# Performance work log

Hardware: AMD Instinct MI355X
Metric: run time of the kernel (lower is better)

Reference implementation:

```python
import jax, jax.numpy as jnp
import numpy as np

D_MODEL = 512
NUM_HEADS = 8
HEAD_DIM = D_MODEL // NUM_HEADS
WINDOW = 64


def setup_inputs() -> dict:
    key = jax.random.key(0)
    ks = jax.random.split(key, 9)
    B, S = 2, 4096
    s = 1.0 / np.sqrt(D_MODEL)
    x = jax.random.normal(ks[0], (B, S, D_MODEL), dtype=jnp.float32)
    Wq = jax.random.uniform(ks[1], (D_MODEL, D_MODEL), jnp.float32, -s, s)
    bq = jax.random.uniform(ks[2], (D_MODEL,), jnp.float32, -s, s)
    Wk = jax.random.uniform(ks[3], (D_MODEL, D_MODEL), jnp.float32, -s, s)
    bk = jax.random.uniform(ks[4], (D_MODEL,), jnp.float32, -s, s)
    Wv = jax.random.uniform(ks[5], (D_MODEL, D_MODEL), jnp.float32, -s, s)
    bv = jax.random.uniform(ks[6], (D_MODEL,), jnp.float32, -s, s)
    Wo = jax.random.uniform(ks[7], (D_MODEL, D_MODEL), jnp.float32, -s, s)
    bo = jax.random.uniform(ks[8], (D_MODEL,), jnp.float32, -s, s)
    return {"x": x, "Wq": Wq, "bq": bq, "Wk": Wk, "bk": bk,
            "Wv": Wv, "bv": bv, "Wo": Wo, "bo": bo}


def reference(x, Wq, bq, Wk, bk, Wv, bv, Wo, bo):
    B, S, _ = x.shape
    # projections (torch Linear: x @ W.T + b)
    q = (x @ Wq.T + bq).reshape(B, S, NUM_HEADS, HEAD_DIM).transpose(0, 2, 1, 3)
    k = (x @ Wk.T + bk).reshape(B, S, NUM_HEADS, HEAD_DIM).transpose(0, 2, 1, 3)
    v = (x @ Wv.T + bv).reshape(B, S, NUM_HEADS, HEAD_DIM).transpose(0, 2, 1, 3)
    scores = jnp.einsum('bhqd,bhkd->bhqk', q, k) / jnp.sqrt(
        jnp.asarray(HEAD_DIM, x.dtype))
    idx = jnp.arange(S)
    local = jnp.abs(idx[None, :] - idx[:, None]) <= WINDOW  # [S,S]
    scores = jnp.where(local[None, None], scores, -jnp.inf)
    attn = jax.nn.softmax(scores, axis=-1)
    out = jnp.einsum('bhqk,bhkd->bhqd', attn, v)
    out = out.transpose(0, 2, 1, 3).reshape(B, S, D_MODEL)
    return out @ Wo.T + bo
```

## Files before the change

### kernel.cpp

```cpp
#include <hip/hip_runtime.h>
#include <hip/hip_bf16.h>

typedef __attribute__((ext_vector_type(8))) short short8;
typedef __attribute__((ext_vector_type(4))) short s16x4;
typedef __attribute__((ext_vector_type(4))) float f32x4;

#define S_LEN 4096
#define DM 512
#define NH 8
#define HD 64
#define NB 2

__device__ __forceinline__ ushort f2bf(float f) {
    union { float f; unsigned int i; } x; x.f = f;
    unsigned int i = x.i;
    unsigned int r = (i + 0x7fffu + ((i >> 16) & 1u)) >> 16;
    return (ushort)r;
}

__device__ __forceinline__ void gload16(const ushort* g, ushort* l) {
    __builtin_amdgcn_global_load_lds(
        (const __attribute__((address_space(1))) unsigned int*)(g),
        (__attribute__((address_space(3))) unsigned int*)(l),
        16, 0, 0);
}

__device__ __forceinline__ f32x4 mfma16(s16x4 a, s16x4 b, f32x4 c) {
#if __has_builtin(__builtin_amdgcn_mfma_f32_16x16x16bf16_1k)
    return __builtin_amdgcn_mfma_f32_16x16x16bf16_1k(a, b, c, 0, 0, 0);
#else
    f32x4 d;
    asm volatile("v_mfma_f32_16x16x16_bf16 %0, %1, %2, %3"
                 : "=v"(d) : "v"(a), "v"(b), "v"(c));
    return d;
#endif
}

__global__ __launch_bounds__(256) void cvt_all_kernel(
    const float* __restrict__ x,
    const float* __restrict__ s0, const float* __restrict__ s1,
    const float* __restrict__ s2, const float* __restrict__ s3,
    ushort* __restrict__ xb,
    ushort* __restrict__ t0, ushort* __restrict__ t1,
    ushort* __restrict__ t2, ushort* __restrict__ t3)
{
    const float* src;
    ushort* dst;
    size_t i;
    if (blockIdx.x < 2048) {
        src = x; dst = xb;
        i = (size_t)blockIdx.x * 256 + threadIdx.x;
    } else {
        const int wb = blockIdx.x - 2048;
        const int which = wb >> 7;
        src = (which == 0) ? s0 : (which == 1) ? s1 : (which == 2) ? s2 : s3;
        dst = (which == 0) ? t0 : (which == 1) ? t1 : (which == 2) ? t2 : t3;
        i = (size_t)(wb & 127) * 256 + threadIdx.x;
    }
    const float4* s = (const float4*)src;
    float4 a = s[i * 2], b = s[i * 2 + 1];
    short8 o;
    o[0] = (short)f2bf(a.x); o[1] = (short)f2bf(a.y);
    o[2] = (short)f2bf(a.z); o[3] = (short)f2bf(a.w);
    o[4] = (short)f2bf(b.x); o[5] = (short)f2bf(b.y);
    o[6] = (short)f2bf(b.z); o[7] = (short)f2bf(b.w);
    *(short8*)(dst + i * 8) = o;
}

__global__ __launch_bounds__(256) void qkv_proj_kernel(
    const ushort* __restrict__ X,
    const ushort* __restrict__ Wq, const float* __restrict__ bq,
    const ushort* __restrict__ Wk, const float* __restrict__ bk,
    const ushort* __restrict__ Wv, const float* __restrict__ bv,
    ushort* __restrict__ Qws, ushort* __restrict__ Kws, ushort* __restrict__ Vt)
{
    __shared__ __align__(1024) ushort As[128 * 64];
    __shared__ __align__(1024) ushort Bs[128 * 64];

    const int lane = threadIdx.x & 63;
    const int w    = threadIdx.x >> 6;
    const int xcd  = blockIdx.x & 7;
    const int idx  = blockIdx.x >> 3;
    const int tr   = xcd + 8 * (idx / 12);
    const int tc   = idx % 12;
    const int which = tc >> 2;
    const int c0   = (tc & 3) * 128;
    const int r0   = tr * 128;

    const ushort* W    = (which == 0) ? Wq : (which == 1) ? Wk : Wv;
    const float*  bias = (which == 0) ? bq : (which == 1) ? bk : bv;

    const int lr = lane & 15;
    const int lg = lane >> 4;
    const int wr = w >> 1, wc = w & 1;
    const int ldrow = lane >> 3;
    const int ldcol = (lane & 7) * 8;

    f32x4 acc[4][4] = {};
    for (int ks = 0; ks < 8; ks++) {
        const int k0 = ks * 64;
        if (ks) __syncthreads();
        const ushort* gA = X + (size_t)(r0 + ldrow) * DM + k0 + ldcol;
        const ushort* gB = W + (size_t)(c0 + ldrow) * DM + k0 + ldcol;
#pragma unroll
        for (int j = 0; j < 4; j++) {
            const int ch = w * 4 + j;
            gload16(gA + (size_t)ch * 8 * DM, As + ch * 512);
            gload16(gB + (size_t)ch * 8 * DM, Bs + ch * 512);
        }
        __syncthreads();

#pragma unroll
        for (int kk = 0; kk < 2; kk++) {
            const int koff = kk * 32 + lg * 8;
            short8 a[4], b[4];
#pragma unroll
            for (int m = 0; m < 4; m++)
                a[m] = *(const short8*)(As + (wr * 64 + 16 * m + lr) * 64 + koff);
#pragma unroll
            for (int n = 0; n < 4; n++)
                b[n] = *(const short8*)(Bs + (wc * 64 + 16 * n + lr) * 64 + koff);
#pragma unroll
            for (int m = 0; m < 4; m++)
#pragma unroll
                for (int n = 0; n < 4; n++)
                    acc[m][n] = __builtin_amdgcn_mfma_f32_16x16x32_bf16(a[m], b[n], acc[m][n], 0, 0, 0);
        }
    }

#pragma unroll
    for (int n = 0; n < 4; n++) {
        const int c = c0 + wc * 64 + 16 * n + lr;
        const float bb = bias[c];
        const int h = c >> 6, d = c & 63;
#pragma unroll
        for (int m = 0; m < 4; m++) {
#pragma unroll
            for (int r = 0; r < 4; r++) {
                const int row = r0 + wr * 64 + 16 * m + 4 * lg + r;
                const int bidx = row >> 12;
                const int s = row & (S_LEN - 1);
                const ushort o = f2bf(acc[m][n][r] + bb);
                if (which == 2) {
                    Vt[((size_t)(bidx * NH + h) * HD + d) * S_LEN + s] = o;
                } else {
                    ushort* dst = (which == 0) ? Qws : Kws;
                    dst[((size_t)(bidx * NH + h) * S_LEN + s) * HD + d] = o;
                }
            }
        }
    }
}

__global__ __launch_bounds__(256) void attn_kernel(
    const ushort* __restrict__ Qws, const ushort* __restrict__ Kws,
    const ushort* __restrict__ Vt, ushort* __restrict__ AO)
{
    __shared__ __align__(1024) ushort Ks[192 * 64];
    __shared__ __align__(1024) ushort Vs[64 * 192];

    const int x   = blockIdx.x;
    const int xcd = x & 7;
    const int idx = x >> 3;
    const int bh  = xcd * 2 + (idx >> 6);
    const int qb  = idx & 63;
    const int w   = threadIdx.x >> 6;
    const int lane = threadIdx.x & 63;
    const int lr = lane & 15;
    const int lg = lane >> 4;

    const ushort* Qh = Qws + (size_t)bh * S_LEN * HD;
    const ushort* Kh = Kws + (size_t)bh * S_LEN * HD;
    const ushort* Vh = Vt  + (size_t)bh * HD * S_LEN;

    const int q0 = qb * 64 + w * 16;
    const int kstart = qb * 64 - 64;

#pragma unroll
    for (int i = 0; i < 6; i++) {
        const int sb = w * 384 + i * 64;
        const int s = sb + lane;
        const int row = s >> 3;
        const int g = (s & 7) ^ (row & 7);
        int rg = kstart + row;
        rg = (rg < 0) ? 0 : (rg >= S_LEN ? S_LEN - 1 : rg);
        gload16(Kh + (size_t)rg * HD + g * 8, Ks + sb * 8);
    }
#pragma unroll
    for (int i = 0; i < 6; i++) {
        const int sb = w * 384 + i * 64;
        const int s = sb + lane;
        const int row = s / 24;
        const int sr = s - row * 24;
        const int cr = sr ^ (row & 7);
        int cg = kstart + cr * 8;
        cg = (cg < 0) ? 0 : (cg > S_LEN - 8 ? S_LEN - 8 : cg);
        gload16(Vh + (size_t)row * S_LEN + cg, Vs + sb * 8);
    }

    short8 qa[2];
#pragma unroll
    for (int kk = 0; kk < 2; kk++)
        qa[kk] = *(const short8*)(Qh + (size_t)(q0 + lr) * HD + kk * 32 + lg * 8);

    __syncthreads();

    const int swz = (lr & 7) << 3;

    f32x4 sc[12];
#pragma unroll
    for (int ct = 0; ct < 12; ct++) {
        sc[ct] = f32x4{0.f, 0.f, 0.f, 0.f};
        const int base = (ct * 16 + lr) * 64;
        short8 kb0 = *(const short8*)(Ks + (base + ((0  + lg * 8) ^ swz)));
        short8 kb1 = *(const short8*)(Ks + (base + ((32 + lg * 8) ^ swz)));
        sc[ct] = __builtin_amdgcn_mfma_f32_16x16x32_bf16(kb0, qa[0], sc[ct], 0, 0, 0);
        sc[ct] = __builtin_amdgcn_mfma_f32_16x16x32_bf16(kb1, qa[1], sc[ct], 0, 0, 0);
    }

    const float scale2 = 0.18033688f;
    const int qi = q0 + lr;
    float sum = 0.f;
#pragma unroll
    for (int ct = 0; ct < 12; ct++) {
#pragma unroll
        for (int r = 0; r < 4; r++) {
            const int j = kstart + ct * 16 + 4 * lg + r;
            const bool valid = (j >= 0) && (j < S_LEN) && (qi - j <= 64) && (j - qi <= 64);
            const float p = valid ? exp2f(sc[ct][r] * scale2) : 0.f;
            sc[ct][r] = p;
            sum += p;
        }
    }
    sum += __shfl_xor(sum, 16);
    sum += __shfl_xor(sum, 32);
    const float inv = 1.0f / sum;

    s16x4 pb[12];
#pragma unroll
    for (int ct = 0; ct < 12; ct++) {
        pb[ct][0] = (short)f2bf(sc[ct][0]);
        pb[ct][1] = (short)f2bf(sc[ct][1]);
        pb[ct][2] = (short)f2bf(sc[ct][2]);
        pb[ct][3] = (short)f2bf(sc[ct][3]);
    }

    f32x4 po[4] = {};
#pragma unroll
    for (int ct = 0; ct < 12; ct++) {
        const int k0 = ct * 16 + 4 * lg;
        const int sub = k0 & 7;
        const int ch = k0 >> 3;
#pragma unroll
        for (int n = 0; n < 4; n++) {
            const int d = 16 * n + lr;
            s16x4 va = *(const s16x4*)(Vs + d * 192 + 8 * (ch ^ (lr & 7)) + sub);
            po[n] = mfma16(va, pb[ct], po[n]);
        }
    }

    const int b = bh >> 3, h = bh & 7;
    ushort* aorow = AO + ((size_t)(b * S_LEN + q0 + lr)) * DM + h * HD;
#pragma unroll
    for (int n = 0; n < 4; n++) {
        uint2 u;
        u.x = (uint)f2bf(po[n][0] * inv) | ((uint)f2bf(po[n][1] * inv) << 16);
        u.y = (uint)f2bf(po[n][2] * inv) | ((uint)f2bf(po[n][3] * inv) << 16);
        *(uint2*)(aorow + 16 * n + 4 * lg) = u;
    }
}

__global__ __launch_bounds__(256) void out_proj_kernel(
    const ushort* __restrict__ AO, const ushort* __restrict__ Wo,
    const float* __restrict__ bo, float* __restrict__ Out)
{
    __shared__ __align__(1024) ushort As[128 * 64];
    __shared__ __align__(1024) ushort Bs[128 * 64];

    const int lane = threadIdx.x & 63;
    const int w    = threadIdx.x >> 6;
    const int xcd  = blockIdx.x & 7;
    const int idx  = blockIdx.x >> 3;
    const int tr   = xcd + 8 * (idx >> 2);
    const int tc   = idx & 3;
    const int c0   = tc * 128;
    const int r0   = tr * 128;
    const int lr = lane & 15;
    const int lg = lane >> 4;
    const int wr = w >> 1, wc = w & 1;
    const int ldrow = lane >> 3;
    const int ldcol = (lane & 7) * 8;

    f32x4 acc[4][4] = {};
    for (int ks = 0; ks < 8; ks++) {
        const int k0 = ks * 64;
        if (ks) __syncthreads();
        const ushort* gA = AO + (size_t)(r0 + ldrow) * DM + k0 + ldcol;
        const ushort* gB = Wo + (size_t)(c0 + ldrow) * DM + k0 + ldcol;
#pragma unroll
        for (int j = 0; j < 4; j++) {
            const int ch = w * 4 + j;
            gload16(gA + (size_t)ch * 8 * DM, As + ch * 512);
            gload16(gB + (size_t)ch * 8 * DM, Bs + ch * 512);
        }
        __syncthreads();

#pragma unroll
        for (int kk = 0; kk < 2; kk++) {
            const int koff = kk * 32 + lg * 8;
            short8 a[4], b[4];
#pragma unroll
            for (int m = 0; m < 4; m++)
                a[m] = *(const short8*)(As + (wr * 64 + 16 * m + lr) * 64 + koff);
#pragma unroll
            for (int n = 0; n < 4; n++)
                b[n] = *(const short8*)(Bs + (wc * 64 + 16 * n + lr) * 64 + koff);
#pragma unroll
            for (int m = 0; m < 4; m++)
#pragma unroll
                for (int n = 0; n < 4; n++)
                    acc[m][n] = __builtin_amdgcn_mfma_f32_16x16x32_bf16(a[m], b[n], acc[m][n], 0, 0, 0);
        }
    }

#pragma unroll
    for (int n = 0; n < 4; n++) {
        const int c = c0 + wc * 64 + 16 * n + lr;
        const float bb = bo[c];
#pragma unroll
        for (int m = 0; m < 4; m++) {
#pragma unroll
            for (int r = 0; r < 4; r++) {
                const int row = r0 + wr * 64 + 16 * m + 4 * lg + r;
                Out[(size_t)row * DM + c] = acc[m][n][r] + bb;
            }
        }
    }
}

extern "C" void kernel_launch(void* const* d_in, const int* in_sizes, int n_in,
                              void* d_out, int out_size, void* d_ws, size_t ws_size,
                              hipStream_t stream) {
    const float* x  = (const float*)d_in[0];
    const float* Wq = (const float*)d_in[1];
    const float* bq = (const float*)d_in[2];
    const float* Wk = (const float*)d_in[3];
    const float* bk = (const float*)d_in[4];
    const float* Wv = (const float*)d_in[5];
    const float* bv = (const float*)d_in[6];
    const float* Wo = (const float*)d_in[7];
    const float* bo = (const float*)d_in[8];
    float* out = (float*)d_out;

    const size_t XE = (size_t)NB * S_LEN * DM;
    const size_t WE = (size_t)DM * DM;

    ushort* Xb  = (ushort*)d_ws;
    ushort* Wqb = Xb + XE;
    ushort* Wkb = Wqb + WE;
    ushort* Wvb = Wkb + WE;
    ushort* Wob = Wvb + WE;
    ushort* Qws = Wob + WE;
    ushort* Kws = Qws + XE;
    ushort* Vt  = Kws + XE;
    ushort* AO  = Vt + XE;

    cvt_all_kernel<<<2560, 256, 0, stream>>>(x, Wq, Wk, Wv, Wo, Xb, Wqb, Wkb, Wvb, Wob);
    qkv_proj_kernel<<<768, 256, 0, stream>>>(Xb, Wqb, bq, Wkb, bk, Wvb, bv, Qws, Kws, Vt);
    attn_kernel<<<1024, 256, 0, stream>>>(Qws, Kws, Vt, AO);
    out_proj_kernel<<<256, 256, 0, stream>>>(AO, Wob, bo, out);
}
```

Measured before the change: 65.16 us.

## Fuse Q/K/V projections per tile so each X tile feeds all three weights

Each QKV projection block now computes a 128x64 output tile for Q, K and V together, loading the X tile once and reusing it across three weight tiles. The grid shrinks from 768 to 512 blocks. The V transpose store now packs four consecutive sequence values into one 8-byte write instead of scalar stores. The aim is to cut redundant X loads and improve write coalescing for Vt. In exchange there are fewer blocks, more accumulator registers (24 f32x4) and more LDS per block.

New measurement: 60.93 us. 1.07x faster.

```diff
diff --git a/kernel.cpp b/kernel.cpp
--- a/kernel.cpp
+++ b/kernel.cpp
@@ -75,77 +75,92 @@
     ushort* __restrict__ Qws, ushort* __restrict__ Kws, ushort* __restrict__ Vt)
 {
     __shared__ __align__(1024) ushort As[128 * 64];
-    __shared__ __align__(1024) ushort Bs[128 * 64];
+    __shared__ __align__(1024) ushort Bs[3][64 * 64];
 
     const int lane = threadIdx.x & 63;
     const int w    = threadIdx.x >> 6;
     const int xcd  = blockIdx.x & 7;
     const int idx  = blockIdx.x >> 3;
-    const int tr   = xcd + 8 * (idx / 12);
-    const int tc   = idx % 12;
-    const int which = tc >> 2;
-    const int c0   = (tc & 3) * 128;
+    const int tc   = idx & 7;
+    const int tr   = xcd + 8 * (idx >> 3);
+    const int c0   = tc * 64;
     const int r0   = tr * 128;
 
-    const ushort* W    = (which == 0) ? Wq : (which == 1) ? Wk : Wv;
-    const float*  bias = (which == 0) ? bq : (which == 1) ? bk : bv;
+    const ushort* Wm[3] = { Wq, Wk, Wv };
+    const float*  bm[3] = { bq, bk, bv };
 
     const int lr = lane & 15;
     const int lg = lane >> 4;
-    const int wr = w >> 1, wc = w & 1;
     const int ldrow = lane >> 3;
     const int ldcol = (lane & 7) * 8;
 
-    f32x4 acc[4][4] = {};
+    f32x4 acc[3][2][4] = {};
     for (int ks = 0; ks < 8; ks++) {
         const int k0 = ks * 64;
         if (ks) __syncthreads();
         const ushort* gA = X + (size_t)(r0 + ldrow) * DM + k0 + ldcol;
-        const ushort* gB = W + (size_t)(c0 + ldrow) * DM + k0 + ldcol;
 #pragma unroll
         for (int j = 0; j < 4; j++) {
             const int ch = w * 4 + j;
             gload16(gA + (size_t)ch * 8 * DM, As + ch * 512);
-            gload16(gB + (size_t)ch * 8 * DM, Bs + ch * 512);
+        }
+#pragma unroll
+        for (int j = 0; j < 6; j++) {
+            const int q = w * 6 + j;
+            const int mat = q >> 3, ch = q & 7;
+            gload16(Wm[mat] + (size_t)(c0 + ch * 8 + ldrow) * DM + k0 + ldcol,
+                    &Bs[mat][ch * 512]);
         }
         __syncthreads();
 
 #pragma unroll
         for (int kk = 0; kk < 2; kk++) {
             const int koff = kk * 32 + lg * 8;
-            short8 a[4], b[4];
-#pragma unroll
-            for (int m = 0; m < 4; m++)
-                a[m] = *(const short8*)(As + (wr * 64 + 16 * m + lr) * 64 + koff);
-#pragma unroll
-            for (int n = 0; n < 4; n++)
-                b[n] = *(const short8*)(Bs + (wc * 64 + 16 * n + lr) * 64 + koff);
-#pragma unroll
-            for (int m = 0; m < 4; m++)
+            short8 a[2], b[3][4];
+#pragma unroll
+            for (int m = 0; m < 2; m++)
+                a[m] = *(const short8*)(As + (w * 32 + 16 * m + lr) * 64 + koff);
+#pragma unroll
+            for (int mat = 0; mat < 3; mat++)
 #pragma unroll
                 for (int n = 0; n < 4; n++)
-                    acc[m][n] = __builtin_amdgcn_mfma_f32_16x16x32_bf16(a[m], b[n], acc[m][n], 0, 0, 0);
-        }
-    }
-
-#pragma unroll
-    for (int n = 0; n < 4; n++) {
-        const int c = c0 + wc * 64 + 16 * n + lr;
-        const float bb = bias[c];
-        const int h = c >> 6, d = c & 63;
-#pragma unroll
-        for (int m = 0; m < 4; m++) {
-#pragma unroll
-            for (int r = 0; r < 4; r++) {
-                const int row = r0 + wr * 64 + 16 * m + 4 * lg + r;
-                const int bidx = row >> 12;
-                const int s = row & (S_LEN - 1);
-                const ushort o = f2bf(acc[m][n][r] + bb);
-                if (which == 2) {
-                    Vt[((size_t)(bidx * NH + h) * HD + d) * S_LEN + s] = o;
+                    b[mat][n] = *(const short8*)(&Bs[mat][(16 * n + lr) * 64 + koff]);
+#pragma unroll
+            for (int mat = 0; mat < 3; mat++)
+#pragma unroll
+                for (int m = 0; m < 2; m++)
+#pragma unroll
+                    for (int n = 0; n < 4; n++)
+                        acc[mat][m][n] = __builtin_amdgcn_mfma_f32_16x16x32_bf16(
+                            a[m], b[mat][n], acc[mat][m][n], 0, 0, 0);
+        }
+    }
+
+#pragma unroll
+    for (int mat = 0; mat < 3; mat++) {
+#pragma unroll
+        for (int n = 0; n < 4; n++) {
+            const int c = c0 + 16 * n + lr;
+            const float bb = bm[mat][c];
+            const int h = c >> 6, d = c & 63;
+#pragma unroll
+            for (int m = 0; m < 2; m++) {
+                const int row0 = r0 + w * 32 + 16 * m + 4 * lg;
+                const int bidx = row0 >> 12;
+                const int s0 = row0 & (S_LEN - 1);
+                if (mat == 2) {
+                    uint2 u;
+                    u.x = (uint)f2bf(acc[2][m][n][0] + bb) |
+                          ((uint)f2bf(acc[2][m][n][1] + bb) << 16);
+                    u.y = (uint)f2bf(acc[2][m][n][2] + bb) |
+                          ((uint)f2bf(acc[2][m][n][3] + bb) << 16);
+                    *(uint2*)(Vt + ((size_t)(bidx * NH + h) * HD + d) * S_LEN + s0) = u;
                 } else {
-                    ushort* dst = (which == 0) ? Qws : Kws;
-                    dst[((size_t)(bidx * NH + h) * S_LEN + s) * HD + d] = o;
+                    ushort* dst = (mat == 0) ? Qws : Kws;
+#pragma unroll
+                    for (int r = 0; r < 4; r++)
+                        dst[((size_t)(bidx * NH + h) * S_LEN + s0 + r) * HD + d] =
+                            f2bf(acc[mat][m][n][r] + bb);
                 }
             }
         }
@@ -366,7 +381,7 @@
     ushort* AO  = Vt + XE;
 
     cvt_all_kernel<<<2560, 256, 0, stream>>>(x, Wq, Wk, Wv, Wo, Xb, Wqb, Wkb, Wvb, Wob);
-    qkv_proj_kernel<<<768, 256, 0, stream>>>(Xb, Wqb, bq, Wkb, bk, Wvb, bv, Qws, Kws, Vt);
+    qkv_proj_kernel<<<512, 256, 0, stream>>>(Xb, Wqb, bq, Wkb, bk, Wvb, bv, Qws, Kws, Vt);
     attn_kernel<<<1024, 256, 0, stream>>>(Qws, Kws, Vt, AO);
     out_proj_kernel<<<256, 256, 0, stream>>>(AO, Wob, bo, out);
 }
```
